# Kernel optimization log

Hardware: AMD Instinct MI355X
Metric: run time of the kernel (lower is better)

The kernel has to match this reference:

```python
import jax, jax.numpy as jnp
import numpy as np

B, C, N, F_IN = 8, 5, 512, 768
H, D_HID, D_OUT = 4, 128, 64
NEG_SLOPE = 0.2


def _gat_layer(h, mask, W, a_l, a_r, b, apply_relu):
    # h: [B,N,Fin], mask: [B,N,N] bool (mask[b,i,j]=True means edge i->j)
    Bn, Nn, _ = h.shape
    Hh, Dd = a_l.shape
    feat = (h @ W).reshape(Bn, Nn, Hh, Dd)              # [B,N,H,D]
    el = jnp.einsum('bnhd,hd->bnh', feat, a_l)          # src scores
    er = jnp.einsum('bnhd,hd->bnh', feat, a_r)          # dst scores
    e = jax.nn.leaky_relu(el[:, :, None, :] + er[:, None, :, :], NEG_SLOPE)  # [B,src,dst,H]
    m = mask[..., None]
    e = jnp.where(m, e, jnp.finfo(e.dtype).min)
    emax = jnp.max(e, axis=1, keepdims=True)
    p = jnp.where(m, jnp.exp(e - emax), 0.0)
    s = jnp.sum(p, axis=1, keepdims=True)
    alpha = p / jnp.maximum(s, 1e-9)                    # edge softmax over incoming edges per dst
    out = jnp.einsum('bijh,bihd->bjhd', alpha, feat)    # aggregate src features to dst
    out = out + b.reshape(1, 1, Hh, Dd)
    if apply_relu:
        out = jax.nn.relu(out)
    return out                                           # [B,N,H,D]


def setup_inputs() -> dict:
    key = jax.random.key(0)
    ks = jax.random.split(key, 16)
    x = jax.random.normal(ks[0], (B, C, N, F_IN), dtype=jnp.float32)
    adj = (jax.random.uniform(ks[1], (B, C, N, N)) < 0.1).astype(jnp.float32)
    node_nums = jnp.full((B,), N, dtype=jnp.int32)
    s = 0.02
    W0 = jax.random.normal(ks[2], (C, F_IN, H * D_HID)) * s
    al0 = jax.random.normal(ks[3], (C, H, D_HID)) * s
    ar0 = jax.random.normal(ks[4], (C, H, D_HID)) * s
    b0 = jnp.zeros((C, H * D_HID), jnp.float32)
    W1 = jax.random.normal(ks[5], (C, H * D_HID, H * D_HID)) * s
    al1 = jax.random.normal(ks[6], (C, H, D_HID)) * s
    ar1 = jax.random.normal(ks[7], (C, H, D_HID)) * s
    b1 = jnp.zeros((C, H * D_HID), jnp.float32)
    W2 = jax.random.normal(ks[8], (C, H * D_HID, H * D_OUT)) * s
    al2 = jax.random.normal(ks[9], (C, H, D_OUT)) * s
    ar2 = jax.random.normal(ks[10], (C, H, D_OUT)) * s
    b2 = jnp.zeros((C, H * D_OUT), jnp.float32)
    return dict(x=x, adj=adj, W0=W0, al0=al0, ar0=ar0, b0=b0,
                W1=W1, al1=al1, ar1=ar1, b1=b1,
                W2=W2, al2=al2, ar2=ar2, b2=b2, node_nums=node_nums)


def reference(x, adj, W0, al0, ar0, b0, W1, al1, ar1, b1, W2, al2, ar2, b2, node_nums):
    # Original concatenates per-batch node slices and takes channel 0 features only.
    h0 = x[:, 0]                       # [B,N,F_IN]
    logits_all = []
    for c in range(C):
        mask = adj[:, c] > 0           # [B,N,N]
        h = _gat_layer(h0, mask, W0[c], al0[c], ar0[c], b0[c].reshape(H, D_HID), True).reshape(B, N, H * D_HID)
        h = _gat_layer(h, mask, W1[c], al1[c], ar1[c], b1[c].reshape(H, D_HID), True).reshape(B, N, H * D_HID)
        out = _gat_layer(h, mask, W2[c], al2[c], ar2[c], b2[c].reshape(H, D_OUT), False).mean(axis=2)  # [B,N,D_OUT]
        logits_all.append(out)
    return jnp.concatenate(logits_all, axis=-1)  # [B,N,C*D_OUT]
```

## Files before the change

### kernel.cpp

```cpp
#include <hip/hip_runtime.h>

typedef unsigned int uint;
typedef unsigned short ushort_t;
typedef __attribute__((ext_vector_type(8))) short short8;
typedef __attribute__((ext_vector_type(4))) float f32x4;

#define NB 8
#define NC 5
#define NN 512
#define FIN 768
#define NH 4
#define MT 4096

__device__ __forceinline__ float b2f(ushort_t u){ uint x = ((uint)u)<<16; return __builtin_bit_cast(float, x); }
__device__ __forceinline__ ushort_t f2b(float f){
  uint u = __builtin_bit_cast(uint, f);
  u += 0x7FFFu + ((u>>16)&1u);
  return (ushort_t)(u>>16);
}
__device__ __forceinline__ ushort_t f2b_fast(float f){
  uint u = __builtin_bit_cast(uint, f);
  return (ushort_t)((u + 0x8000u)>>16);
}

#if __has_builtin(__builtin_amdgcn_cvt_pk_bf16_f32)
typedef __bf16 bf16x2 __attribute__((ext_vector_type(2)));
__device__ __forceinline__ uint pk2(float a, float b){
  return __builtin_bit_cast(uint, __builtin_amdgcn_cvt_pk_bf16_f32(a, b));
}
#else
__device__ __forceinline__ uint pk2(float a, float b){
  return (uint)f2b_fast(a) | ((uint)f2b_fast(b) << 16);
}
#endif

#define GLL16(gp, lp) __builtin_amdgcn_global_load_lds( \
    (const __attribute__((address_space(1))) void*)(gp), \
    (__attribute__((address_space(3))) void*)(lp), 16, 0, 0)

__global__ __launch_bounds__(256) void prep(const float* __restrict__ x, ushort_t* __restrict__ h0b,
                                            const float* __restrict__ W0, ushort_t* __restrict__ Wt0,
                                            const float* __restrict__ W1, ushort_t* __restrict__ Wt1,
                                            const float* __restrict__ W2, ushort_t* __restrict__ Wt2,
                                            const float* __restrict__ adj, uint* __restrict__ adjB){
  __shared__ float tile[32][33];
  int bid = blockIdx.x, t = threadIdx.x;
  if (bid < 3072){
    int tid = bid*256 + t;
    int row = tid/192, q = tid%192;
    int b = row >> 9, n = row & 511;
    float4 v = *(const float4*)(x + ((size_t)(b*NC)*NN + n)*FIN + q*4);
    ushort4 o; o.x = f2b(v.x); o.y = f2b(v.y); o.z = f2b(v.z); o.w = f2b(v.w);
    *(ushort4*)(h0b + (size_t)row*FIN + q*4) = o;
  } else if (bid < 6912){
    const float* W; ushort_t* Wt; int K, N, c, x0, y0;
    if (bid < 4992){ int l = bid-3072; K=768; N=512; W=W0; Wt=Wt0; c=l/384; int r=l%384; x0=r%16; y0=r/16; }
    else if (bid < 6272){ int l = bid-4992; K=512; N=512; W=W1; Wt=Wt1; c=l/256; int r=l%256; x0=r%16; y0=r/16; }
    else { int l = bid-6272; K=512; N=256; W=W2; Wt=Wt2; c=l/128; int r=l%128; x0=r%8; y0=r/8; }
    int n0 = x0*32, k0 = y0*32;
    int tx = t & 31, ty = t >> 5;
    const float* Wp = W + (size_t)c*K*N;
    ushort_t* Wtp = Wt + (size_t)c*K*N;
    #pragma unroll
    for (int r=0;r<4;r++) tile[ty+r*8][tx] = Wp[(size_t)(k0+ty+r*8)*N + n0+tx];
    __syncthreads();
    #pragma unroll
    for (int r=0;r<4;r++) Wtp[(size_t)(n0+ty+r*8)*K + k0+tx] = f2b(tile[tx][ty+r*8]);
  } else {
    int l = bid - 6912;
    int iw = l & 15, zz = l >> 4;
    const float* ap = adj + (size_t)zz*NN*NN + (size_t)iw*32*NN;
    uint w0 = 0, w1 = 0;
    #pragma unroll 8
    for (int q=0;q<32;q++){
      if (ap[(size_t)q*NN + t]       > 0.f) w0 |= (1u<<q);
      if (ap[(size_t)q*NN + t + 256] > 0.f) w1 |= (1u<<q);
    }
    adjB[((size_t)zz*16 + iw)*512 + t]       = w0;
    adjB[((size_t)zz*16 + iw)*512 + t + 256] = w1;
  }
}

template<int DH>
__global__ __launch_bounds__(256) void gemm_tn(const ushort_t* __restrict__ A,
                                               const ushort_t* __restrict__ Bt,
                                               ushort_t* __restrict__ Ob,
                                               const float* __restrict__ al, const float* __restrict__ ar,
                                               float* __restrict__ el, float* __restrict__ E1, float* __restrict__ E2,
                                               float* __restrict__ er, float* __restrict__ R1, float* __restrict__ R2,
                                               int K, long a_cs, long b_cs){
  constexpr int DT = NH*DH;
  __shared__ __align__(16) char smem[128*136*2];
  __shared__ float als_s[128], ars_s[128];
  ushort_t* As = (ushort_t*)smem;
  ushort_t* Bs = As + 128*32;
  ushort_t* St = (ushort_t*)smem;
  int c = blockIdx.z;
  const ushort_t* Ap = A + (size_t)c*a_cs;
  const ushort_t* Bp = Bt + (size_t)c*b_cs;
  int m0 = blockIdx.y*128, n0 = blockIdx.x*128;
  int t = threadIdx.x, lane = t & 63, w = t >> 6;
  int l15 = lane & 15, quad = lane >> 4;
  int wm = (w & 1)*64, wn = (w >> 1)*64;
  if (t < 128){
    als_s[t] = al[(size_t)c*NH*DH + n0 + t];
    ars_s[t] = ar[(size_t)c*NH*DH + n0 + t];
  }
  f32x4 acc[4][4] = {};
  for (int k0 = 0; k0 < K; k0 += 32){
    __syncthreads();
    {
      int i = t;
      GLL16(Ap + (size_t)(m0 + (i>>2))*K + k0 + (i&3)*8, As + (size_t)(w*64)*8);
      GLL16(Bp + (size_t)(n0 + (i>>2))*K + k0 + (i&3)*8, Bs + (size_t)(w*64)*8);
      i = t + 256;
      GLL16(Ap + (size_t)(m0 + (i>>2))*K + k0 + (i&3)*8, As + (size_t)(w*64 + 256)*8);
      GLL16(Bp + (size_t)(n0 + (i>>2))*K + k0 + (i&3)*8, Bs + (size_t)(w*64 + 256)*8);
    }
    __syncthreads();
    short8 af[4], bfr[4];
    #pragma unroll
    for (int im=0; im<4; im++) af[im] = *(const short8*)(As + (size_t)(wm + im*16 + l15)*32 + quad*8);
    #pragma unroll
    for (int in=0; in<4; in++) bfr[in] = *(const short8*)(Bs + (size_t)(wn + in*16 + l15)*32 + quad*8);
    #pragma unroll
    for (int im=0; im<4; im++)
      #pragma unroll
      for (int in=0; in<4; in++)
        acc[im][in] = __builtin_amdgcn_mfma_f32_16x16x32_bf16(af[im], bfr[in], acc[im][in], 0, 0, 0);
  }
  __syncthreads();
  #pragma unroll
  for (int im=0; im<4; im++)
    #pragma unroll
    for (int in=0; in<4; in++){
      int n = wn + in*16 + l15;
      #pragma unroll
      for (int r=0; r<4; r++){
        int m = wm + im*16 + quad*4 + r;
        St[(size_t)n*136 + m] = f2b(acc[im][in][r]);
      }
    }
  __syncthreads();
  {
    int n_loc = t >> 1, half = t & 1;
    const ushort_t* srcp = St + (size_t)n_loc*136 + half*64;
    ushort_t* dstc = Ob + (size_t)c*MT*DT;
    #pragma unroll
    for (int q=0;q<8;q++){
      size_t g = (size_t)(m0>>3) + half*8 + q;
      *(short8*)(dstc + (g*DT + n0 + n_loc)*8) = *(const short8*)(srcp + q*8);
    }
  }
  {
    int m = t >> 1, half = t & 1;
    float sl = 0.f, sr = 0.f;
    const ushort_t* stp = St + (size_t)(half*64)*136 + m;
    #pragma unroll 8
    for (int nn=0; nn<64; nn++){
      float f = b2f(stp[(size_t)nn*136]);
      int n = half*64 + nn;
      sl += f*als_s[n]; sr += f*ars_s[n];
    }
    size_t base = (size_t)c*NH*MT;
    if (DH == 128){
      sl += __shfl_xor(sl, 1); sr += __shfl_xor(sr, 1);
      size_t idx = base + (size_t)(n0>>7)*MT + m0 + m;
      if (half == 0){ el[idx]=sl; E1[idx]=__expf(sl); E2[idx]=__expf(0.2f*sl); }
      else          { er[idx]=sr; R1[idx]=__expf(sr); R2[idx]=__expf(0.2f*sr); }
    } else {
      size_t idx = base + (size_t)((n0>>6)+half)*MT + m0 + m;
      el[idx]=sl; E1[idx]=__expf(sl); E2[idx]=__expf(0.2f*sl);
      er[idx]=sr; R1[idx]=__expf(sr); R2[idx]=__expf(0.2f*sr);
    }
  }
}

template<int DH, int RELU>
__global__ __launch_bounds__(256,5) void agg(const ushort_t* __restrict__ featB,
                                             const uint* __restrict__ adjB,
                                             const float* __restrict__ el, const float* __restrict__ E1,
                                             const float* __restrict__ E2,
                                             const float* __restrict__ er, const float* __restrict__ R1,
                                             const float* __restrict__ R2,
                                             const float* __restrict__ bias,
                                             ushort_t* __restrict__ outp){
  constexpr int DT = NH*DH;
  constexpr int BN = DH/16;
  __shared__ __align__(16) ushort_t Fs[2][4*DH*8];
  __shared__ float el_s[512], E1_s[512], E2_s[512];
  __shared__ uint Ms[16*64];
  int bid = blockIdx.x;
  int g = bid % 160, jt = bid / 160;
  int c = g>>5, b = (g>>2)&7, h = g&3;
  int zz = b*NC + c;
  int j0 = jt*64;
  int t = threadIdx.x, lane = t&63, w = t>>6, l15 = lane&15, quad = lane>>4;
  size_t eb = (size_t)(c*NH + h)*MT + b*NN;
  const ushort_t* fBc = featB + ((size_t)(c*512 + b*64)*DT + h*DH)*8;
  el_s[t] = el[eb + t]; el_s[t+256] = el[eb + t+256];
  E1_s[t] = E1[eb + t]; E1_s[t+256] = E1[eb + t+256];
  E2_s[t] = E2[eb + t]; E2_s[t+256] = E2[eb + t+256];
  #pragma unroll
  for (int k=0;k<4;k++){
    int idx = k*256 + t;
    Ms[idx] = adjB[((size_t)zz*16 + (idx>>6))*512 + j0 + (idx&63)];
  }
  int jme = j0 + w*16 + l15;
  float erv = er[eb + jme];
  float R1v = R1[eb + jme];
  float R2v = R2[eb + jme];
  short8 onesv;
  #pragma unroll
  for (int q=0;q<8;q++) onesv[q] = (short)0x3F80;
  f32x4 acc[BN] = {};
  f32x4 accs = {0.f,0.f,0.f,0.f};
  #pragma unroll
  for (int part=0; part<DH/64; part++)
    GLL16(fBc + (size_t)w*DT*8 + part*512 + lane*8, &Fs[0][w*(DH*8) + part*512]);
  __syncthreads();
  for (int ic = 0; ic < 16; ic++){
    int buf = ic & 1;
    if (ic < 15){
      #pragma unroll
      for (int part=0; part<DH/64; part++)
        GLL16(fBc + (size_t)((ic+1)*4+w)*DT*8 + part*512 + lane*8, &Fs[buf^1][w*(DH*8) + part*512]);
    }
    int i0c = ic*32;
    uint mby = (Ms[ic*64 + w*16 + l15] >> (quad*8)) & 0xFFu;
    float4 ea  = *(const float4*)&el_s[i0c + quad*8];
    float4 eb4 = *(const float4*)&el_s[i0c + quad*8 + 4];
    float4 x1a = *(const float4*)&E1_s[i0c + quad*8];
    float4 x1b = *(const float4*)&E1_s[i0c + quad*8 + 4];
    float4 x2a = *(const float4*)&E2_s[i0c + quad*8];
    float4 x2b = *(const float4*)&E2_s[i0c + quad*8 + 4];
    float ev[8]  = {ea.x,ea.y,ea.z,ea.w,eb4.x,eb4.y,eb4.z,eb4.w};
    float e1v[8] = {x1a.x,x1a.y,x1a.z,x1a.w,x1b.x,x1b.y,x1b.z,x1b.w};
    float e2v[8] = {x2a.x,x2a.y,x2a.z,x2a.w,x2b.x,x2b.y,x2b.z,x2b.w};
    float pv[8];
    #pragma unroll
    for (int q=0;q<8;q++){
      float s  = ev[q] + erv;
      float Ei = (s > 0.f) ? e1v[q] : e2v[q];
      float Rv = (s > 0.f) ? R1v : R2v;
      float p  = Ei*Rv;
      pv[q] = ((mby>>q)&1u) ? p : 0.f;
    }
    uint4 pw;
    pw.x = pk2(pv[0], pv[1]); pw.y = pk2(pv[2], pv[3]);
    pw.z = pk2(pv[4], pv[5]); pw.w = pk2(pv[6], pv[7]);
    short8 af = __builtin_bit_cast(short8, pw);
    accs = __builtin_amdgcn_mfma_f32_16x16x32_bf16(af, onesv, accs, 0, 0, 0);
    #pragma unroll
    for (int half=0; half<2; half++){
      short8 bfr[BN/2];
      #pragma unroll
      for (int in=0; in<BN/2; in++)
        bfr[in] = *(const short8*)&Fs[buf][quad*(DH*8) + ((half*(BN/2)+in)*16 + l15)*8];
      #pragma unroll
      for (int in=0; in<BN/2; in++)
        acc[half*(BN/2)+in] = __builtin_amdgcn_mfma_f32_16x16x32_bf16(af, bfr[in], acc[half*(BN/2)+in], 0, 0, 0);
    }
    __syncthreads();
  }
  ushort_t* op = outp + ((size_t)c*MT + b*NN + j0 + w*16)*DT + h*DH;
  float bv[BN];
  #pragma unroll
  for (int in=0; in<BN; in++) bv[in] = bias[(size_t)c*DT + h*DH + in*16 + l15];
  #pragma unroll
  for (int r=0; r<4; r++){
    int jr = quad*4 + r;
    float sinv = 1.f / fmaxf(accs[r], 1e-9f);
    #pragma unroll
    for (int in=0; in<BN; in++){
      float o = acc[in][r]*sinv + bv[in];
      if (RELU) o = fmaxf(o, 0.f);
      op[(size_t)jr*DT + in*16 + l15] = f2b_fast(o);
    }
  }
}

__global__ __launch_bounds__(256) void meank(const ushort_t* __restrict__ h2, float* __restrict__ outp){
  int tid = blockIdx.x*256 + threadIdx.x;
  if (tid >= MT*NC*64) return;
  int d = tid & 63; int r = tid >> 6; int c = r % NC; int m = r / NC;
  const ushort_t* p = h2 + ((size_t)c*MT + m)*256 + d;
  float s = 0.25f*(b2f(p[0]) + b2f(p[64]) + b2f(p[128]) + b2f(p[192]));
  outp[(size_t)m*(NC*64) + c*64 + d] = s;
}

extern "C" void kernel_launch(void* const* d_in, const int* in_sizes, int n_in,
                              void* d_out, int out_size, void* d_ws, size_t ws_size,
                              hipStream_t stream){
  const float* x   = (const float*)d_in[0];
  const float* adj = (const float*)d_in[1];
  const float* W0  = (const float*)d_in[2];
  const float* al0 = (const float*)d_in[3];
  const float* ar0 = (const float*)d_in[4];
  const float* b0  = (const float*)d_in[5];
  const float* W1  = (const float*)d_in[6];
  const float* al1 = (const float*)d_in[7];
  const float* ar1 = (const float*)d_in[8];
  const float* b1  = (const float*)d_in[9];
  const float* W2  = (const float*)d_in[10];
  const float* al2 = (const float*)d_in[11];
  const float* ar2 = (const float*)d_in[12];
  const float* b2  = (const float*)d_in[13];

  ushort_t* h0b  = (ushort_t*)d_ws;
  ushort_t* Wt0  = h0b  + (size_t)MT*FIN;
  ushort_t* Wt1  = Wt0  + (size_t)5*512*768;
  ushort_t* Wt2  = Wt1  + (size_t)5*512*512;
  ushort_t* featB= Wt2  + (size_t)5*256*512;
  ushort_t* hnat = featB+ (size_t)5*(size_t)MT*512;
  uint*     adjB = (uint*)(hnat + (size_t)5*(size_t)MT*512);
  float*    elp  = (float*)(adjB + (size_t)40*16*512);
  float*    E1p  = elp + (size_t)NC*NH*MT;
  float*    E2p  = E1p + (size_t)NC*NH*MT;
  float*    erp  = E2p + (size_t)NC*NH*MT;
  float*    R1p  = erp + (size_t)NC*NH*MT;
  float*    R2p  = R1p + (size_t)NC*NH*MT;

  prep<<<7552, 256, 0, stream>>>(x, h0b, W0, Wt0, W1, Wt1, W2, Wt2, adj, adjB);

  gemm_tn<128><<<dim3(4,32,5), 256, 0, stream>>>(h0b, Wt0, featB, al0, ar0,
                                                 elp, E1p, E2p, erp, R1p, R2p,
                                                 768, 0L, (long)512*768);
  agg<128,1><<<1280, 256, 0, stream>>>(featB, adjB, elp, E1p, E2p, erp, R1p, R2p, b0, hnat);
  gemm_tn<128><<<dim3(4,32,5), 256, 0, stream>>>(hnat, Wt1, featB, al1, ar1,
                                                 elp, E1p, E2p, erp, R1p, R2p,
                                                 512, (long)MT*512, (long)512*512);
  agg<128,1><<<1280, 256, 0, stream>>>(featB, adjB, elp, E1p, E2p, erp, R1p, R2p, b1, hnat);
  gemm_tn<64><<<dim3(2,32,5), 256, 0, stream>>>(hnat, Wt2, featB, al2, ar2,
                                                elp, E1p, E2p, erp, R1p, R2p,
                                                512, (long)MT*512, (long)256*512);
  agg<64,0><<<1280, 256, 0, stream>>>(featB, adjB, elp, E1p, E2p, erp, R1p, R2p, b2, hnat);

  meank<<<5120, 256, 0, stream>>>(hnat, (float*)d_out);
}
```

Measured before the change: 300.3 us.

## Stage agg feature chunks in large LDS buffers and fuse head-mean into final agg

The agg kernel's per-chunk double-buffered LDS pipeline is replaced by a staged scheme. Each stage loads a 32KB block of feature cells into LDS and then runs several MFMA steps between barriers, which cuts the number of syncs per chunk. Occupancy is lowered to 3 blocks per SM to make room for the larger buffer. The separate mean kernel is removed: the final agg atomically adds 0.25*output into the zero-initialized output, with the zeroing done by extra blocks in prep. The cost is less load/compute overlap within a block, fewer resident blocks, and float atomics on the output.

```diff
diff --git a/kernel.cpp b/kernel.cpp
--- a/kernel.cpp
+++ b/kernel.cpp
@@ -42,7 +42,8 @@
                                             const float* __restrict__ W0, ushort_t* __restrict__ Wt0,
                                             const float* __restrict__ W1, ushort_t* __restrict__ Wt1,
                                             const float* __restrict__ W2, ushort_t* __restrict__ Wt2,
-                                            const float* __restrict__ adj, uint* __restrict__ adjB){
+                                            const float* __restrict__ adj, uint* __restrict__ adjB,
+                                            float* __restrict__ dout){
   __shared__ float tile[32][33];
   int bid = blockIdx.x, t = threadIdx.x;
   if (bid < 3072){
@@ -66,7 +67,7 @@
     __syncthreads();
     #pragma unroll
     for (int r=0;r<4;r++) Wtp[(size_t)(n0+ty+r*8)*K + k0+tx] = f2b(tile[tx][ty+r*8]);
-  } else {
+  } else if (bid < 7552){
     int l = bid - 6912;
     int iw = l & 15, zz = l >> 4;
     const float* ap = adj + (size_t)zz*NN*NN + (size_t)iw*32*NN;
@@ -78,6 +79,11 @@
     }
     adjB[((size_t)zz*16 + iw)*512 + t]       = w0;
     adjB[((size_t)zz*16 + iw)*512 + t + 256] = w1;
+  } else {
+    int l = bid - 7552;
+    float4 z = {0.f,0.f,0.f,0.f};
+    float4* dp = (float4*)dout + (size_t)l*512;
+    dp[t] = z; dp[t+256] = z;
   }
 }
 
@@ -176,18 +182,23 @@
   }
 }
 
-template<int DH, int RELU>
-__global__ __launch_bounds__(256,5) void agg(const ushort_t* __restrict__ featB,
+template<int DH, int RELU, int FINAL>
+__global__ __launch_bounds__(256,3) void agg(const ushort_t* __restrict__ featB,
                                              const uint* __restrict__ adjB,
                                              const float* __restrict__ el, const float* __restrict__ E1,
                                              const float* __restrict__ E2,
                                              const float* __restrict__ er, const float* __restrict__ R1,
                                              const float* __restrict__ R2,
                                              const float* __restrict__ bias,
-                                             ushort_t* __restrict__ outp){
+                                             ushort_t* __restrict__ outp,
+                                             float* __restrict__ dout){
   constexpr int DT = NH*DH;
   constexpr int BN = DH/16;
-  __shared__ __align__(16) ushort_t Fs[2][4*DH*8];
+  constexpr int CELLS = 32768/(DH*16);
+  constexpr int STAGES = 64/CELLS;
+  constexpr int STEPS = CELLS/4;
+  constexpr int PARTS = (DH*8)/512;
+  __shared__ __align__(16) ushort_t Fs[CELLS*DH*8];
   __shared__ float el_s[512], E1_s[512], E2_s[512];
   __shared__ uint Ms[16*64];
   int bid = blockIdx.x;
@@ -215,78 +226,85 @@
   for (int q=0;q<8;q++) onesv[q] = (short)0x3F80;
   f32x4 acc[BN] = {};
   f32x4 accs = {0.f,0.f,0.f,0.f};
-  #pragma unroll
-  for (int part=0; part<DH/64; part++)
-    GLL16(fBc + (size_t)w*DT*8 + part*512 + lane*8, &Fs[0][w*(DH*8) + part*512]);
-  __syncthreads();
-  for (int ic = 0; ic < 16; ic++){
-    int buf = ic & 1;
-    if (ic < 15){
-      #pragma unroll
-      for (int part=0; part<DH/64; part++)
-        GLL16(fBc + (size_t)((ic+1)*4+w)*DT*8 + part*512 + lane*8, &Fs[buf^1][w*(DH*8) + part*512]);
-    }
-    int i0c = ic*32;
-    uint mby = (Ms[ic*64 + w*16 + l15] >> (quad*8)) & 0xFFu;
-    float4 ea  = *(const float4*)&el_s[i0c + quad*8];
-    float4 eb4 = *(const float4*)&el_s[i0c + quad*8 + 4];
-    float4 x1a = *(const float4*)&E1_s[i0c + quad*8];
-    float4 x1b = *(const float4*)&E1_s[i0c + quad*8 + 4];
-    float4 x2a = *(const float4*)&E2_s[i0c + quad*8];
-    float4 x2b = *(const float4*)&E2_s[i0c + quad*8 + 4];
-    float ev[8]  = {ea.x,ea.y,ea.z,ea.w,eb4.x,eb4.y,eb4.z,eb4.w};
-    float e1v[8] = {x1a.x,x1a.y,x1a.z,x1a.w,x1b.x,x1b.y,x1b.z,x1b.w};
-    float e2v[8] = {x2a.x,x2a.y,x2a.z,x2a.w,x2b.x,x2b.y,x2b.z,x2b.w};
-    float pv[8];
-    #pragma unroll
-    for (int q=0;q<8;q++){
-      float s  = ev[q] + erv;
-      float Ei = (s > 0.f) ? e1v[q] : e2v[q];
-      float Rv = (s > 0.f) ? R1v : R2v;
-      float p  = Ei*Rv;
-      pv[q] = ((mby>>q)&1u) ? p : 0.f;
-    }
-    uint4 pw;
-    pw.x = pk2(pv[0], pv[1]); pw.y = pk2(pv[2], pv[3]);
-    pw.z = pk2(pv[4], pv[5]); pw.w = pk2(pv[6], pv[7]);
-    short8 af = __builtin_bit_cast(short8, pw);
-    accs = __builtin_amdgcn_mfma_f32_16x16x32_bf16(af, onesv, accs, 0, 0, 0);
-    #pragma unroll
-    for (int half=0; half<2; half++){
-      short8 bfr[BN/2];
-      #pragma unroll
-      for (int in=0; in<BN/2; in++)
-        bfr[in] = *(const short8*)&Fs[buf][quad*(DH*8) + ((half*(BN/2)+in)*16 + l15)*8];
-      #pragma unroll
-      for (int in=0; in<BN/2; in++)
-        acc[half*(BN/2)+in] = __builtin_amdgcn_mfma_f32_16x16x32_bf16(af, bfr[in], acc[half*(BN/2)+in], 0, 0, 0);
-    }
-    __syncthreads();
-  }
-  ushort_t* op = outp + ((size_t)c*MT + b*NN + j0 + w*16)*DT + h*DH;
+  for (int sg = 0; sg < STAGES; sg++){
+    __syncthreads();
+    #pragma unroll
+    for (int u = 0; u < CELLS/4; u++){
+      int cell = w*(CELLS/4) + u;
+      #pragma unroll
+      for (int part = 0; part < PARTS; part++)
+        GLL16(fBc + (size_t)(sg*CELLS + cell)*DT*8 + part*512 + lane*8,
+              Fs + (size_t)cell*(DH*8) + part*512);
+    }
+    __syncthreads();
+    #pragma unroll
+    for (int st = 0; st < STEPS; st++){
+      int i0c = sg*(CELLS*8) + st*32;
+      uint mby = (Ms[(i0c>>5)*64 + w*16 + l15] >> (quad*8)) & 0xFFu;
+      float4 ea  = *(const float4*)&el_s[i0c + quad*8];
+      float4 eb4 = *(const float4*)&el_s[i0c + quad*8 + 4];
+      float4 x1a = *(const float4*)&E1_s[i0c + quad*8];
+      float4 x1b = *(const float4*)&E1_s[i0c + quad*8 + 4];
+      float4 x2a = *(const float4*)&E2_s[i0c + quad*8];
+      float4 x2b = *(const float4*)&E2_s[i0c + quad*8 + 4];
+      float ev[8]  = {ea.x,ea.y,ea.z,ea.w,eb4.x,eb4.y,eb4.z,eb4.w};
+      float e1v[8] = {x1a.x,x1a.y,x1a.z,x1a.w,x1b.x,x1b.y,x1b.z,x1b.w};
+      float e2v[8] = {x2a.x,x2a.y,x2a.z,x2a.w,x2b.x,x2b.y,x2b.z,x2b.w};
+      float pv[8];
+      #pragma unroll
+      for (int q=0;q<8;q++){
+        float s  = ev[q] + erv;
+        float Ei = (s > 0.f) ? e1v[q] : e2v[q];
+        float Rv = (s > 0.f) ? R1v : R2v;
+        float p  = Ei*Rv;
+        pv[q] = ((mby>>q)&1u) ? p : 0.f;
+      }
+      uint4 pw;
+      pw.x = pk2(pv[0], pv[1]); pw.y = pk2(pv[2], pv[3]);
+      pw.z = pk2(pv[4], pv[5]); pw.w = pk2(pv[6], pv[7]);
+      short8 af = __builtin_bit_cast(short8, pw);
+      accs = __builtin_amdgcn_mfma_f32_16x16x32_bf16(af, onesv, accs, 0, 0, 0);
+      #pragma unroll
+      for (int half=0; half<2; half++){
+        short8 bfr[BN/2];
+        #pragma unroll
+        for (int in=0; in<BN/2; in++)
+          bfr[in] = *(const short8*)&Fs[(size_t)(st*4+quad)*(DH*8) + ((half*(BN/2)+in)*16 + l15)*8];
+        #pragma unroll
+        for (int in=0; in<BN/2; in++)
+          acc[half*(BN/2)+in] = __builtin_amdgcn_mfma_f32_16x16x32_bf16(af, bfr[in], acc[half*(BN/2)+in], 0, 0, 0);
+      }
+    }
+  }
   float bv[BN];
   #pragma unroll
   for (int in=0; in<BN; in++) bv[in] = bias[(size_t)c*DT + h*DH + in*16 + l15];
-  #pragma unroll
-  for (int r=0; r<4; r++){
-    int jr = quad*4 + r;
-    float sinv = 1.f / fmaxf(accs[r], 1e-9f);
-    #pragma unroll
-    for (int in=0; in<BN; in++){
-      float o = acc[in][r]*sinv + bv[in];
-      if (RELU) o = fmaxf(o, 0.f);
-      op[(size_t)jr*DT + in*16 + l15] = f2b_fast(o);
-    }
-  }
-}
-
-__global__ __launch_bounds__(256) void meank(const ushort_t* __restrict__ h2, float* __restrict__ outp){
-  int tid = blockIdx.x*256 + threadIdx.x;
-  if (tid >= MT*NC*64) return;
-  int d = tid & 63; int r = tid >> 6; int c = r % NC; int m = r / NC;
-  const ushort_t* p = h2 + ((size_t)c*MT + m)*256 + d;
-  float s = 0.25f*(b2f(p[0]) + b2f(p[64]) + b2f(p[128]) + b2f(p[192]));
-  outp[(size_t)m*(NC*64) + c*64 + d] = s;
+  if (!FINAL){
+    ushort_t* op = outp + ((size_t)c*MT + b*NN + j0 + w*16)*DT + h*DH;
+    #pragma unroll
+    for (int r=0; r<4; r++){
+      int jr = quad*4 + r;
+      float sinv = 1.f / fmaxf(accs[r], 1e-9f);
+      #pragma unroll
+      for (int in=0; in<BN; in++){
+        float o = acc[in][r]*sinv + bv[in];
+        if (RELU) o = fmaxf(o, 0.f);
+        op[(size_t)jr*DT + in*16 + l15] = f2b_fast(o);
+      }
+    }
+  } else {
+    float* dp = dout + ((size_t)b*NN + j0 + w*16)*(NC*64) + c*64;
+    #pragma unroll
+    for (int r=0; r<4; r++){
+      int jr = quad*4 + r;
+      float sinv = 1.f / fmaxf(accs[r], 1e-9f);
+      #pragma unroll
+      for (int in=0; in<BN; in++){
+        float o = acc[in][r]*sinv + bv[in];
+        atomicAdd(dp + (size_t)jr*(NC*64) + in*16 + l15, 0.25f*o);
+      }
+    }
+  }
 }
 
 extern "C" void kernel_launch(void* const* d_in, const int* in_sizes, int n_in,
@@ -320,21 +338,20 @@
   float*    erp  = E2p + (size_t)NC*NH*MT;
   float*    R1p  = erp + (size_t)NC*NH*MT;
   float*    R2p  = R1p + (size_t)NC*NH*MT;
-
-  prep<<<7552, 256, 0, stream>>>(x, h0b, W0, Wt0, W1, Wt1, W2, Wt2, adj, adjB);
+  float*    dout = (float*)d_out;
+
+  prep<<<8192, 256, 0, stream>>>(x, h0b, W0, Wt0, W1, Wt1, W2, Wt2, adj, adjB, dout);
 
   gemm_tn<128><<<dim3(4,32,5), 256, 0, stream>>>(h0b, Wt0, featB, al0, ar0,
                                                  elp, E1p, E2p, erp, R1p, R2p,
                                                  768, 0L, (long)512*768);
-  agg<128,1><<<1280, 256, 0, stream>>>(featB, adjB, elp, E1p, E2p, erp, R1p, R2p, b0, hnat);
+  agg<128,1,0><<<1280, 256, 0, stream>>>(featB, adjB, elp, E1p, E2p, erp, R1p, R2p, b0, hnat, dout);
   gemm_tn<128><<<dim3(4,32,5), 256, 0, stream>>>(hnat, Wt1, featB, al1, ar1,
                                                  elp, E1p, E2p, erp, R1p, R2p,
                                                  512, (long)MT*512, (long)512*512);
-  agg<128,1><<<1280, 256, 0, stream>>>(featB, adjB, elp, E1p, E2p, erp, R1p, R2p, b1, hnat);
+  agg<128,1,0><<<1280, 256, 0, stream>>>(featB, adjB, elp, E1p, E2p, erp, R1p, R2p, b1, hnat, dout);
   gemm_tn<64><<<dim3(2,32,5), 256, 0, stream>>>(hnat, Wt2, featB, al2, ar2,
                                                 elp, E1p, E2p, erp, R1p, R2p,
                                                 512, (long)MT*512, (long)256*512);
-  agg<64,0><<<1280, 256, 0, stream>>>(featB, adjB, elp, E1p, E2p, erp, R1p, R2p, b2, hnat);
-
-  meank<<<5120, 256, 0, stream>>>(hnat, (float*)d_out);
-}
+  agg<64,0,1><<<1280, 256, 0, stream>>>(featB, adjB, elp, E1p, E2p, erp, R1p, R2p, b2, hnat, dout);
+}
```

After: 321.3 us. 1.07x slower.
